# Kernel tuning notes

Hardware: AMD Instinct MI355X
Metric: run time of the kernel (lower is better)

## Reference

```python
import jax, jax.numpy as jnp
import numpy as np

ORDER = 12      # Coef_num in the original
BLOCK = 1024
N_FFT = 2046    # torch.stft(n_fft=2046) -> 1024 onesided bins
HOP = 511       # torch default n_fft // 4
WORN = 1024
G1, G2 = 0.92, 0.6


def burg_lpc(y):
    """Burg's method LPC (exactly librosa.lpc), vectorized over blocks. y: [B, N] -> [B, ORDER+1]."""
    ar = jnp.zeros((y.shape[0], ORDER + 1), y.dtype).at[:, 0].set(1.0)
    f = y[:, 1:]
    b = y[:, :-1]
    den = jnp.sum(f * f, -1) + jnp.sum(b * b, -1)
    for i in range(ORDER):
        k = -2.0 * jnp.sum(b * f, -1) / den                     # reflection coeff [B]
        js = np.arange(1, i + 2)
        ar = ar.at[:, js].set(ar[:, js] + k[:, None] * ar[:, i - js + 1])
        f_new = f + k[:, None] * b
        b = b + k[:, None] * f
        f = f_new
        den = (1.0 - k * k) * den - b[:, -1] ** 2 - f[:, 0] ** 2
        f = f[:, 1:]
        b = b[:, :-1]
    return ar


def perceptual_weights(y):
    """Stacked |freqz| weight matrix [n_blocks*11, 1024], matching the original append order."""
    n_blocks = y.shape[0] // BLOCK
    yb = y[: n_blocks * BLOCK].reshape(n_blocks, BLOCK)
    lpc = burg_lpc(yb)[:, :ORDER]                               # original drops coeff index 12
    j = np.arange(ORDER)
    a1 = (lpc * (G1 ** j)).astype(jnp.complex64)                # denominator coeffs (bandwidth-expanded)
    a2 = (lpc * (G2 ** j)).astype(jnp.complex64)                # numerator coeffs
    omega = jnp.pi * jnp.arange(WORN) / WORN                    # freqz worN=1024 digital freqs
    E = jnp.exp(-1j * omega[:, None] * j[None, :]).astype(jnp.complex64)   # [F, 12]
    # freqz is called inside the k1 loop: at step k1 only coeffs 0..k1 are filled -> triangular mask
    M = jnp.asarray(j[None, :] <= np.arange(1, ORDER)[:, None], jnp.complex64)  # [11, 12]
    num = jnp.einsum('bj,kj,fj->bkf', a2, M, E)
    den = jnp.einsum('bj,kj,fj->bkf', a1, M, E)
    return jnp.abs(num / den).reshape(n_blocks * (ORDER - 1), WORN)


def stft_mag(x):
    """torch.stft(x, n_fft=2046, center=True, reflect pad, rect window, onesided) magnitude -> [1024, n_frames]."""
    pad = N_FFT // 2
    xp = jnp.pad(x, (pad, pad), mode='reflect')
    n_frames = 1 + x.shape[0] // HOP
    idx = jnp.arange(n_frames)[:, None] * HOP + jnp.arange(N_FFT)[None, :]
    frames = xp[idx]                                            # [n_frames, 2046]
    return jnp.abs(jnp.fft.rfft(frames, axis=1)).T              # [1024, n_frames]


def setup_inputs() -> dict:
    key = jax.random.key(0)
    kx, ky = jax.random.split(key)
    L = 2048 * 1024
    x = jax.random.normal(kx, (L,), dtype=jnp.float32)
    y = jax.random.normal(ky, (L,), dtype=jnp.float32)
    return {"x": x, "y": y}


def reference(x, y):
    W = jax.lax.stop_gradient(perceptual_weights(y))            # original computes weights on detached numpy
    Sx = stft_mag(x)
    Sy = stft_mag(y)
    mse = jnp.mean((Sx - Sy) ** 2, axis=1)                      # [1024] per-frequency-bin MSE over frames
    return jnp.mean(mse[None, :] / W)                           # broadcast over [n_blocks*11, 1024]
```

## Files before the change

kernel.cpp:

```cpp
#include <hip/hip_runtime.h>
#include <hip/hip_bf16.h>

#define PI_D 3.14159265358979323846
#define L_TOTAL 2097152
#define NFRAMES 4105
#define NBLK    4108
#define MROWS_P 8216
#define MPAD    8320
#define KP      512
#define NDIM    2048
#define PSTRIDE 8224


#define FRAMES_BLOCKS 2080
#define BASIS_BLOCKS  512
#define SARR_BLOCKS   17
#define BURG_BLOCKS   512
#define PREP_BLOCKS   (FRAMES_BLOCKS + BASIS_BLOCKS + SARR_BLOCKS + BURG_BLOCKS)

typedef __attribute__((ext_vector_type(8))) short short8;
typedef __attribute__((ext_vector_type(4))) short short4v;
typedef __attribute__((ext_vector_type(4))) float floatx4;

typedef __attribute__((address_space(1))) void gvoid_as1;
typedef __attribute__((address_space(3))) void lvoid_as3;

__device__ __forceinline__ void gld_lds16(const void* g, void* l) {
    __builtin_amdgcn_global_load_lds((gvoid_as1*)g, (lvoid_as3*)l, 16, 0, 0);
}

__device__ __forceinline__ float b2f(short v) {
    unsigned int u = ((unsigned int)(unsigned short)v) << 16;
    return __uint_as_float(u);
}

__device__ __forceinline__ float xorall(float v) {
    v += __shfl_xor(v, 1, 64);
    v += __shfl_xor(v, 2, 64);
    v += __shfl_xor(v, 4, 64);
    v += __shfl_xor(v, 8, 64);
    v += __shfl_xor(v, 16, 64);
    v += __shfl_xor(v, 32, 64);
    return v;
}

__device__ __forceinline__ float wave_reduce(float v) {
    v += __shfl_down(v, 32, 64);
    v += __shfl_down(v, 16, 64);
    v += __shfl_down(v, 8, 64);
    v += __shfl_down(v, 4, 64);
    v += __shfl_down(v, 2, 64);
    v += __shfl_down(v, 1, 64);
    return v;
}

__device__ __forceinline__ void frames_body(int bid, int tid,
                                            const float* __restrict__ x,
                                            const float* __restrict__ y,
                                            __hip_bfloat16* __restrict__ A) {
    const int ci = bid * 256 + tid;
    const int rb = ci >> 10;
    const int kc = (ci >> 4) & 63;
    const int rowIn = ci & 15;
    const int row = rb * 16 + rowIn;
    __hip_bfloat16 tmp[8];
    if (row < MROWS_P) {
        const int b = row >> 1;
        const float* src = (row & 1) ? y : x;
        const int base = b * 511 + kc * 8 - 1023;
#pragma unroll
        for (int e = 0; e < 8; e++) {
            const int n = kc * 8 + e;
            float v = 0.f;
            if (n < 511) {
                int p = base + e;
                if (p < 0) p = -p;
                else if (p >= L_TOTAL) p = 2 * L_TOTAL - 2 - p;
                v = src[p];
            }
            tmp[e] = __float2bfloat16(v);
        }
    } else {
#pragma unroll
        for (int e = 0; e < 8; e++) tmp[e] = __float2bfloat16(0.f);
    }
    *(short8*)((char*)A + (size_t)ci * 16) = *(short8*)tmp;
}

__device__ __forceinline__ void basis_body(int bid, int tid,
                                           __hip_bfloat16* __restrict__ Bt) {
    const int ci = bid * 256 + tid;
    const int rb = ci >> 10;
    const int kc = (ci >> 4) & 63;
    const int rowIn = ci & 15;
    const int row = rb * 16 + rowIn;
    const int f = row >> 1;
    const bool isSin = row & 1;
    __hip_bfloat16 tmp[8];
#pragma unroll
    for (int e = 0; e < 8; e++) {
        const int n = kc * 8 + e;
        float v = 0.f;
        if (n < 511) {
            const int m = (f * n) % 2046;
            const float ang = (float)m * (float)(PI_D / 1023.0);
            float s, c;
            __sincosf(ang, &s, &c);
            v = isSin ? -s : c;
        }
        tmp[e] = __float2bfloat16(v);
    }
    *(short8*)((char*)Bt + (size_t)ci * 16) = *(short8*)tmp;
}

__device__ __forceinline__ void sarr_body(int bid, int tid,
                                          const float* __restrict__ x,
                                          const float* __restrict__ y,
                                          float4* __restrict__ S) {
    const int b = bid * 256 + tid;
    int p0 = 511 * b - 1023;
    int p1 = p0 + 1;
    int m0 = (p0 < 0) ? -p0 : ((p0 >= L_TOTAL) ? 2 * L_TOTAL - 2 - p0 : p0);
    int m1 = (p1 < 0) ? -p1 : ((p1 >= L_TOTAL) ? 2 * L_TOTAL - 2 - p1 : p1);
    S[b] = make_float4(x[m0], x[m1], y[m0], y[m1]);
}

__device__ __forceinline__ void burg_body(int bid, int tid,
                                          const float* __restrict__ y,
                                          float* __restrict__ ar_out,
                                          float* __restrict__ wsf) {
    if (bid < 8) wsf[bid * 256 + tid] = 0.f;

    const int lane = tid & 63;
    const int wid = tid >> 6;
    const int blk = bid * 4 + wid;
    const float4* yb4 = (const float4*)(y + (size_t)blk * 1024) + lane * 4;

    float t[16];
#pragma unroll
    for (int q = 0; q < 4; q++) {
        float4 v = yb4[q];
        t[q * 4 + 0] = v.x; t[q * 4 + 1] = v.y;
        t[q * 4 + 2] = v.z; t[q * 4 + 3] = v.w;
    }
    float b[16], f[16];
#pragma unroll
    for (int r = 0; r < 16; r++) b[r] = t[r];
#pragma unroll
    for (int r = 0; r < 15; r++) f[r] = t[r + 1];
    {
        float nb = __shfl_down(t[0], 1, 64);
        f[15] = (lane == 63) ? 0.f : nb;
        if (lane == 63) b[15] = 0.f;
    }

    float den = 0.f;
#pragma unroll
    for (int r = 0; r < 16; r++) den += f[r] * f[r] + b[r] * b[r];
    den = xorall(den);

    float ar_s[13];
    ar_s[0] = 1.f;
#pragma unroll
    for (int j = 1; j < 13; j++) ar_s[j] = 0.f;

#pragma unroll
    for (int i = 0; i < 12; i++) {
        float num = 0.f;
#pragma unroll
        for (int r = 0; r < 16; r++) num += f[r] * b[r];
        num = xorall(num);
        const float k = -2.f * num / den;

        float fu[16], bu[16];
#pragma unroll
        for (int r = 0; r < 16; r++) {
            fu[r] = f[r] + k * b[r];
            bu[r] = b[r] + k * f[r];
        }
        const float f0 = __shfl(fu[0], 0, 64);
        const int pos = 1022 - i;
        const int L = pos >> 4, S = pos & 15;
        const float blast = __shfl(bu[S], L, 64);

        den = (1.f - k * k) * den - blast * blast - f0 * f0;

        float nf = __shfl_down(fu[0], 1, 64);
#pragma unroll
        for (int r = 0; r < 15; r++) f[r] = fu[r + 1];
        f[15] = (lane == 63) ? 0.f : nf;
#pragma unroll
        for (int r = 0; r < 16; r++) b[r] = bu[r];
        if (lane == L) b[S] = 0.f;

        float tmp[13];
#pragma unroll
        for (int js = 1; js <= i + 1; js++) tmp[js] = ar_s[js] + k * ar_s[i + 1 - js];
#pragma unroll
        for (int js = 1; js <= i + 1; js++) ar_s[js] = tmp[js];
    }

#pragma unroll
    for (int j = 0; j < 12; j++)
        if (lane == j) ar_out[(size_t)blk * 12 + j] = ar_s[j];
}

__global__ __launch_bounds__(256) void prep_kernel(const float* __restrict__ x,
                                                   const float* __restrict__ y,
                                                   __hip_bfloat16* __restrict__ A,
                                                   __hip_bfloat16* __restrict__ Bt,
                                                   float4* __restrict__ S,
                                                   float* __restrict__ ar,
                                                   float* __restrict__ wsf) {
    const int bid = blockIdx.x;
    const int tid = threadIdx.x;
    if (bid < FRAMES_BLOCKS) {
        frames_body(bid, tid, x, y, A);
    } else if (bid < FRAMES_BLOCKS + BASIS_BLOCKS) {
        basis_body(bid - FRAMES_BLOCKS, tid, Bt);
    } else if (bid < FRAMES_BLOCKS + BASIS_BLOCKS + SARR_BLOCKS) {
        sarr_body(bid - FRAMES_BLOCKS - BASIS_BLOCKS, tid, x, y, S);
    } else {
        burg_body(bid - FRAMES_BLOCKS - BASIS_BLOCKS - SARR_BLOCKS, tid, y, ar, wsf);
    }
}

__global__ __launch_bounds__(256) void invw_kernel(const float* __restrict__ ar,
                                                   float* __restrict__ invW) {
    __shared__ float sar[16][12];
    const int tid = threadIdx.x;
    const int f = blockIdx.x * 256 + tid;
    const int b0 = blockIdx.y * 16;
    if (tid < 16 * 12) ((float*)sar)[tid] = ar[(size_t)b0 * 12 + tid];
    __syncthreads();

    const float omega = (float)(PI_D / 1024.0) * (float)f;
    float sw, cw;
    __sincosf(omega, &sw, &cw);

    float acc = 0.f;
#pragma unroll 4
    for (int bb = 0; bb < 16; bb++) {
        float a0 = sar[bb][0];
        float nr = a0, ni = 0.f, dr = a0, di = 0.f;
        float er = 1.f, ei = 0.f;
        float g1p = 1.f, g2p = 1.f;
#pragma unroll
        for (int j = 1; j < 12; j++) {
            float er2 = er * cw + ei * sw;
            float ei2 = ei * cw - er * sw;
            er = er2; ei = ei2;
            g1p *= 0.92f; g2p *= 0.6f;
            float aj = sar[bb][j];
            float a1 = aj * g1p, a2 = aj * g2p;
            nr += a2 * er; ni += a2 * ei;
            dr += a1 * er; di += a1 * ei;
            float D = dr * dr + di * di;
            float Nn = nr * nr + ni * ni;
            acc += D * __builtin_amdgcn_rsqf(D * Nn);
        }
    }
    atomicAdd(&invW[f], acc);
}

__global__ __launch_bounds__(256) void gemm_p_kernel(
    const __hip_bfloat16* __restrict__ A, const __hip_bfloat16* __restrict__ Bt,
    __hip_bfloat16* __restrict__ Pt) {
    __shared__ __align__(16) __hip_bfloat16 Al[128 * 32];
    __shared__ __align__(16) __hip_bfloat16 Bl[128 * 32];

    const int tid = threadIdx.x;
    const int lane = tid & 63;
    const int w = tid >> 6;
    const int wm = w >> 1, wn = w & 1;
    const int q = lane >> 4, l15 = lane & 15;
    const int tileN = blockIdx.x * 128;
    const int tileM = blockIdx.y * 128;

    floatx4 acc[4][4];
#pragma unroll
    for (int i = 0; i < 4; i++)
#pragma unroll
        for (int j = 0; j < 4; j++) acc[i][j] = (floatx4){0.f, 0.f, 0.f, 0.f};

    const int rl = tid & 15;
    const int qq = (tid >> 4) & 3;
    const int gg0 = tid >> 6;
    const char* pA0 = (const char*)A + ((((size_t)(tileM >> 4) + gg0) << 10) + qq * 16 + rl) * 16;
    const char* pA1 = pA0 + (size_t)4 * 16384;
    const char* pB0 = (const char*)Bt + ((((size_t)(tileN >> 4) + gg0) << 10) + qq * 16 + rl) * 16;
    const char* pB1 = pB0 + (size_t)4 * 16384;
    char* AlB = (char*)Al;
    char* BlB = (char*)Bl;

    for (int it = 0; it < KP / 32; it++) {
        gld_lds16(pA0, AlB + tid * 16);
        gld_lds16(pA1, AlB + (tid + 256) * 16);
        gld_lds16(pB0, BlB + tid * 16);
        gld_lds16(pB1, BlB + (tid + 256) * 16);
        pA0 += 1024; pA1 += 1024; pB0 += 1024; pB1 += 1024;
        __syncthreads();

        short8 af[4], bf[4];
#pragma unroll
        for (int sm = 0; sm < 4; sm++)
            af[sm] = *(const short8*)(AlB + (((wm * 4 + sm) * 64 + lane) * 16));
#pragma unroll
        for (int sn = 0; sn < 4; sn++)
            bf[sn] = *(const short8*)(BlB + (((wn * 4 + sn) * 64 + lane) * 16));
#pragma unroll
        for (int sm = 0; sm < 4; sm++)
#pragma unroll
            for (int sn = 0; sn < 4; sn++)
                acc[sm][sn] = __builtin_amdgcn_mfma_f32_16x16x32_bf16(
                    af[sm], bf[sn], acc[sm][sn], 0, 0, 0);
        __syncthreads();
    }

#pragma unroll
    for (int sm = 0; sm < 4; sm++) {
        const int rowBase = tileM + wm * 64 + sm * 16 + q * 4;
        if (rowBase >= MROWS_P) continue;
#pragma unroll
        for (int sn = 0; sn < 4; sn++) {
            const int colG = tileN + wn * 64 + sn * 16 + l15;
            short4v pk;
#pragma unroll
            for (int r = 0; r < 4; r++) {
                __hip_bfloat16 h = __float2bfloat16(acc[sm][sn][r]);
                pk[r] = *(short*)&h;
            }
            *(short4v*)((char*)Pt + ((size_t)colG * PSTRIDE + rowBase) * 2) = pk;
        }
    }
}

__global__ __launch_bounds__(256) void combine_kernel(
    const __hip_bfloat16* __restrict__ Pt,
    const float4* __restrict__ S,
    float* __restrict__ mse_sum) {
    const int tid = threadIdx.x;
    const int lane = tid & 63;
    const int wid = tid >> 6;
    const int f = blockIdx.x * 4 + wid;
    const int ty = blockIdx.y;

    float wc[4], ws[4];
    wc[0] = 1.f; ws[0] = 0.f;
#pragma unroll
    for (int h = 1; h < 4; h++) {
        int m = (511 * h * f) % 2046;
        float s, c;
        __sincosf((float)m * (float)(PI_D / 1023.0), &s, &c);
        wc[h] = c; ws[h] = -s;
    }
    float wtc0, wts0, wtc1, wts1;
    {
        int m = (2044 * f) % 2046;
        float s, c;
        __sincosf((float)m * (float)(PI_D / 1023.0), &s, &c);
        wtc0 = c; wts0 = -s;
        m = (2045 * f) % 2046;
        __sincosf((float)m * (float)(PI_D / 1023.0), &s, &c);
        wtc1 = c; wts1 = -s;
    }

    const __hip_bfloat16* rowRe = Pt + (size_t)(2 * f) * PSTRIDE;
    const __hip_bfloat16* rowIm = rowRe + PSTRIDE;

    float acc = 0.f;
    const int tt0 = ty * 256 + 4 * lane;
    if (tt0 < NFRAMES) {
        short8 re0 = *(const short8*)(rowRe + 2 * tt0);
        short8 re1 = *(const short8*)(rowRe + 2 * tt0 + 8);
        short8 im0 = *(const short8*)(rowIm + 2 * tt0);
        short8 im1 = *(const short8*)(rowIm + 2 * tt0 + 8);
        float4 sT[4];
#pragma unroll
        for (int d = 0; d < 4; d++) sT[d] = S[tt0 + 4 + d];
        float vr[16], vi[16];
#pragma unroll
        for (int j = 0; j < 8; j++) {
            vr[j] = b2f(re0[j]); vr[j + 8] = b2f(re1[j]);
            vi[j] = b2f(im0[j]); vi[j + 8] = b2f(im1[j]);
        }
#pragma unroll
        for (int d = 0; d < 4; d++) {
            const int tt = tt0 + d;
            if (tt >= NFRAMES) break;
            float xr = 0.f, xi = 0.f, yr = 0.f, yi = 0.f;
#pragma unroll
            for (int h = 0; h < 4; h++) {
                const int qx = 2 * d + 2 * h;
                xr += wc[h] * vr[qx] - ws[h] * vi[qx];
                xi += wc[h] * vi[qx] + ws[h] * vr[qx];
                const int qy = qx + 1;
                yr += wc[h] * vr[qy] - ws[h] * vi[qy];
                yi += wc[h] * vi[qy] + ws[h] * vr[qy];
            }
            const float4 sd = sT[d];
            xr += wtc0 * sd.x + wtc1 * sd.y;
            xi += wts0 * sd.x + wts1 * sd.y;
            yr += wtc0 * sd.z + wtc1 * sd.w;
            yi += wts0 * sd.z + wts1 * sd.w;
            float dm = sqrtf(xr * xr + xi * xi) - sqrtf(yr * yr + yi * yi);
            acc += dm * dm;
        }
    }
    acc = xorall(acc);
    if (lane == 0) atomicAdd(&mse_sum[f], acc);
}

__global__ void final_kernel(const float* __restrict__ mse_sum,
                             const float* __restrict__ invW,
                             float* __restrict__ out) {
    __shared__ float red[4];
    const int tid = threadIdx.x;
    float lo = 0.f;
    for (int f = tid; f < 1024; f += 256) lo += mse_sum[f] * invW[f];
    lo = wave_reduce(lo);
    if ((tid & 63) == 0) red[tid >> 6] = lo;
    __syncthreads();
    if (tid == 0) {
        float tot = red[0] + red[1] + red[2] + red[3];
        out[0] = tot * (float)(1.0 / (4105.0 * 22528.0 * 1024.0));
    }
}

extern "C" void kernel_launch(void* const* d_in, const int* in_sizes, int n_in,
                              void* d_out, int out_size, void* d_ws, size_t ws_size,
                              hipStream_t stream) {
    const float* x = (const float*)d_in[0];
    const float* y = (const float*)d_in[1];
    float* out = (float*)d_out;

    float* wsf = (float*)d_ws;
    float* mse_sum = wsf;
    float* invW = wsf + 1024;
    float* ar = wsf + 2048;
    float4* S = (float4*)((char*)d_ws + 106496);
    __hip_bfloat16* Ap = (__hip_bfloat16*)((char*)d_ws + 196608);
    __hip_bfloat16* Bp = (__hip_bfloat16*)((char*)d_ws + 8716288);
    __hip_bfloat16* Pt = (__hip_bfloat16*)((char*)d_ws + 10813440);

    prep_kernel<<<PREP_BLOCKS, 256, 0, stream>>>(x, y, Ap, Bp, S, ar, wsf);
    invw_kernel<<<dim3(4, 128), 256, 0, stream>>>(ar, invW);
    gemm_p_kernel<<<dim3(NDIM / 128, MPAD / 128), 256, 0, stream>>>(Ap, Bp, Pt);
    combine_kernel<<<dim3(256, 17), 256, 0, stream>>>(Pt, S, mse_sum);
    final_kernel<<<1, 256, 0, stream>>>(mse_sum, invW, out);
}
```

Baseline: 145.1 us.

## Merge invW into GEMM launch, fold final reduction into combine, cheapen basis sincos

Fuses the invw kernel into the GEMM launch as extra blocks, and replaces the final reduction kernel with a last-block-done counter pattern inside the combine kernel. Together these cut the launch count from five to three and remove small tail kernels. The basis generator now computes the twiddle factors with one sincos plus a rotation recurrence instead of eight sincos calls. The recurrence can add small rounding drift, but the values are rounded to bf16 anyway. The counter lives in the workspace and is zeroed by prep, so the workspace offsets are shifted to make room for it.

```diff
diff --git a/kernel.cpp b/kernel.cpp
--- a/kernel.cpp
+++ b/kernel.cpp
@@ -10,6 +10,10 @@
 #define KP      512
 #define NDIM    2048
 #define PSTRIDE 8224
+
+#define GEMM_BLOCKS 1040
+#define INVW_BLOCKS 512
+#define COMBINE_BLOCKS (256 * 17)
 
 
 #define FRAMES_BLOCKS 2080
@@ -96,19 +100,21 @@
     const int row = rb * 16 + rowIn;
     const int f = row >> 1;
     const bool isSin = row & 1;
+    const int n0 = kc * 8;
+    const int m0 = (f * n0) % 2046;
+    float s, c, ss, cs;
+    __sincosf((float)m0 * (float)(PI_D / 1023.0), &s, &c);
+    __sincosf((float)f * (float)(PI_D / 1023.0), &ss, &cs);
     __hip_bfloat16 tmp[8];
 #pragma unroll
     for (int e = 0; e < 8; e++) {
-        const int n = kc * 8 + e;
-        float v = 0.f;
-        if (n < 511) {
-            const int m = (f * n) % 2046;
-            const float ang = (float)m * (float)(PI_D / 1023.0);
-            float s, c;
-            __sincosf(ang, &s, &c);
-            v = isSin ? -s : c;
-        }
+        const int n = n0 + e;
+        float v = isSin ? -s : c;
+        if (n >= 511) v = 0.f;
         tmp[e] = __float2bfloat16(v);
+        float c2 = c * cs - s * ss;
+        float s2 = s * cs + c * ss;
+        c = c2; s = s2;
     }
     *(short8*)((char*)Bt + (size_t)ci * 16) = *(short8*)tmp;
 }
@@ -129,7 +135,10 @@
                                           const float* __restrict__ y,
                                           float* __restrict__ ar_out,
                                           float* __restrict__ wsf) {
-    if (bid < 8) wsf[bid * 256 + tid] = 0.f;
+    if (bid < 9) {
+        const int idx = bid * 256 + tid;
+        if (idx < 2080) wsf[idx] = 0.f;
+    }
 
     const int lane = tid & 63;
     const int wid = tid >> 6;
@@ -225,12 +234,82 @@
     }
 }
 
-__global__ __launch_bounds__(256) void invw_kernel(const float* __restrict__ ar,
-                                                   float* __restrict__ invW) {
-    __shared__ float sar[16][12];
-    const int tid = threadIdx.x;
-    const int f = blockIdx.x * 256 + tid;
-    const int b0 = blockIdx.y * 16;
+__device__ __forceinline__ void gemm_body(int bx, int by, int tid, char* smem,
+                                          const __hip_bfloat16* __restrict__ A,
+                                          const __hip_bfloat16* __restrict__ Bt,
+                                          __hip_bfloat16* __restrict__ Pt) {
+    char* AlB = smem;
+    char* BlB = smem + 8192;
+
+    const int lane = tid & 63;
+    const int w = tid >> 6;
+    const int wm = w >> 1, wn = w & 1;
+    const int q = lane >> 4, l15 = lane & 15;
+    const int tileN = bx * 128;
+    const int tileM = by * 128;
+
+    floatx4 acc[4][4];
+#pragma unroll
+    for (int i = 0; i < 4; i++)
+#pragma unroll
+        for (int j = 0; j < 4; j++) acc[i][j] = (floatx4){0.f, 0.f, 0.f, 0.f};
+
+    const int rl = tid & 15;
+    const int qq = (tid >> 4) & 3;
+    const int gg0 = tid >> 6;
+    const char* pA0 = (const char*)A + ((((size_t)(tileM >> 4) + gg0) << 10) + qq * 16 + rl) * 16;
+    const char* pA1 = pA0 + (size_t)4 * 16384;
+    const char* pB0 = (const char*)Bt + ((((size_t)(tileN >> 4) + gg0) << 10) + qq * 16 + rl) * 16;
+    const char* pB1 = pB0 + (size_t)4 * 16384;
+
+    for (int it = 0; it < KP / 32; it++) {
+        gld_lds16(pA0, AlB + tid * 16);
+        gld_lds16(pA1, AlB + (tid + 256) * 16);
+        gld_lds16(pB0, BlB + tid * 16);
+        gld_lds16(pB1, BlB + (tid + 256) * 16);
+        pA0 += 1024; pA1 += 1024; pB0 += 1024; pB1 += 1024;
+        __syncthreads();
+
+        short8 af[4], bf[4];
+#pragma unroll
+        for (int sm = 0; sm < 4; sm++)
+            af[sm] = *(const short8*)(AlB + (((wm * 4 + sm) * 64 + lane) * 16));
+#pragma unroll
+        for (int sn = 0; sn < 4; sn++)
+            bf[sn] = *(const short8*)(BlB + (((wn * 4 + sn) * 64 + lane) * 16));
+#pragma unroll
+        for (int sm = 0; sm < 4; sm++)
+#pragma unroll
+            for (int sn = 0; sn < 4; sn++)
+                acc[sm][sn] = __builtin_amdgcn_mfma_f32_16x16x32_bf16(
+                    af[sm], bf[sn], acc[sm][sn], 0, 0, 0);
+        __syncthreads();
+    }
+
+#pragma unroll
+    for (int sm = 0; sm < 4; sm++) {
+        const int rowBase = tileM + wm * 64 + sm * 16 + q * 4;
+        if (rowBase >= MROWS_P) continue;
+#pragma unroll
+        for (int sn = 0; sn < 4; sn++) {
+            const int colG = tileN + wn * 64 + sn * 16 + l15;
+            short4v pk;
+#pragma unroll
+            for (int r = 0; r < 4; r++) {
+                __hip_bfloat16 h = __float2bfloat16(acc[sm][sn][r]);
+                pk[r] = *(short*)&h;
+            }
+            *(short4v*)((char*)Pt + ((size_t)colG * PSTRIDE + rowBase) * 2) = pk;
+        }
+    }
+}
+
+__device__ __forceinline__ void invw_body(int bid, int tid, char* smem,
+                                          const float* __restrict__ ar,
+                                          float* __restrict__ invW) {
+    float (*sar)[12] = (float(*)[12])smem;
+    const int f = (bid & 3) * 256 + tid;
+    const int b0 = (bid >> 2) * 16;
     if (tid < 16 * 12) ((float*)sar)[tid] = ar[(size_t)b0 * 12 + tid];
     __syncthreads();
 
@@ -263,82 +342,27 @@
     atomicAdd(&invW[f], acc);
 }
 
-__global__ __launch_bounds__(256) void gemm_p_kernel(
+__global__ __launch_bounds__(256) void gemm_invw_kernel(
     const __hip_bfloat16* __restrict__ A, const __hip_bfloat16* __restrict__ Bt,
-    __hip_bfloat16* __restrict__ Pt) {
-    __shared__ __align__(16) __hip_bfloat16 Al[128 * 32];
-    __shared__ __align__(16) __hip_bfloat16 Bl[128 * 32];
-
+    __hip_bfloat16* __restrict__ Pt,
+    const float* __restrict__ ar, float* __restrict__ invW) {
+    __shared__ __align__(16) char smem[16384];
+    const int bid = blockIdx.x;
     const int tid = threadIdx.x;
-    const int lane = tid & 63;
-    const int w = tid >> 6;
-    const int wm = w >> 1, wn = w & 1;
-    const int q = lane >> 4, l15 = lane & 15;
-    const int tileN = blockIdx.x * 128;
-    const int tileM = blockIdx.y * 128;
-
-    floatx4 acc[4][4];
-#pragma unroll
-    for (int i = 0; i < 4; i++)
-#pragma unroll
-        for (int j = 0; j < 4; j++) acc[i][j] = (floatx4){0.f, 0.f, 0.f, 0.f};
-
-    const int rl = tid & 15;
-    const int qq = (tid >> 4) & 3;
-    const int gg0 = tid >> 6;
-    const char* pA0 = (const char*)A + ((((size_t)(tileM >> 4) + gg0) << 10) + qq * 16 + rl) * 16;
-    const char* pA1 = pA0 + (size_t)4 * 16384;
-    const char* pB0 = (const char*)Bt + ((((size_t)(tileN >> 4) + gg0) << 10) + qq * 16 + rl) * 16;
-    const char* pB1 = pB0 + (size_t)4 * 16384;
-    char* AlB = (char*)Al;
-    char* BlB = (char*)Bl;
-
-    for (int it = 0; it < KP / 32; it++) {
-        gld_lds16(pA0, AlB + tid * 16);
-        gld_lds16(pA1, AlB + (tid + 256) * 16);
-        gld_lds16(pB0, BlB + tid * 16);
-        gld_lds16(pB1, BlB + (tid + 256) * 16);
-        pA0 += 1024; pA1 += 1024; pB0 += 1024; pB1 += 1024;
-        __syncthreads();
-
-        short8 af[4], bf[4];
-#pragma unroll
-        for (int sm = 0; sm < 4; sm++)
-            af[sm] = *(const short8*)(AlB + (((wm * 4 + sm) * 64 + lane) * 16));
-#pragma unroll
-        for (int sn = 0; sn < 4; sn++)
-            bf[sn] = *(const short8*)(BlB + (((wn * 4 + sn) * 64 + lane) * 16));
-#pragma unroll
-        for (int sm = 0; sm < 4; sm++)
-#pragma unroll
-            for (int sn = 0; sn < 4; sn++)
-                acc[sm][sn] = __builtin_amdgcn_mfma_f32_16x16x32_bf16(
-                    af[sm], bf[sn], acc[sm][sn], 0, 0, 0);
-        __syncthreads();
-    }
-
-#pragma unroll
-    for (int sm = 0; sm < 4; sm++) {
-        const int rowBase = tileM + wm * 64 + sm * 16 + q * 4;
-        if (rowBase >= MROWS_P) continue;
-#pragma unroll
-        for (int sn = 0; sn < 4; sn++) {
-            const int colG = tileN + wn * 64 + sn * 16 + l15;
-            short4v pk;
-#pragma unroll
-            for (int r = 0; r < 4; r++) {
-                __hip_bfloat16 h = __float2bfloat16(acc[sm][sn][r]);
-                pk[r] = *(short*)&h;
-            }
-            *(short4v*)((char*)Pt + ((size_t)colG * PSTRIDE + rowBase) * 2) = pk;
-        }
+    if (bid < GEMM_BLOCKS) {
+        gemm_body(bid & 15, bid >> 4, tid, smem, A, Bt, Pt);
+    } else {
+        invw_body(bid - GEMM_BLOCKS, tid, smem, ar, invW);
     }
 }
 
 __global__ __launch_bounds__(256) void combine_kernel(
     const __hip_bfloat16* __restrict__ Pt,
     const float4* __restrict__ S,
-    float* __restrict__ mse_sum) {
+    float* __restrict__ mse_sum,
+    const float* __restrict__ invW,
+    int* __restrict__ cnt,
+    float* __restrict__ out) {
     const int tid = threadIdx.x;
     const int lane = tid & 63;
     const int wid = tid >> 6;
@@ -409,21 +433,30 @@
     }
     acc = xorall(acc);
     if (lane == 0) atomicAdd(&mse_sum[f], acc);
-}
-
-__global__ void final_kernel(const float* __restrict__ mse_sum,
-                             const float* __restrict__ invW,
-                             float* __restrict__ out) {
-    __shared__ float red[4];
-    const int tid = threadIdx.x;
-    float lo = 0.f;
-    for (int f = tid; f < 1024; f += 256) lo += mse_sum[f] * invW[f];
-    lo = wave_reduce(lo);
-    if ((tid & 63) == 0) red[tid >> 6] = lo;
+
+    __threadfence();
     __syncthreads();
+    __shared__ int isLast;
     if (tid == 0) {
-        float tot = red[0] + red[1] + red[2] + red[3];
-        out[0] = tot * (float)(1.0 / (4105.0 * 22528.0 * 1024.0));
+        int old = __hip_atomic_fetch_add(cnt, 1, __ATOMIC_ACQ_REL, __HIP_MEMORY_SCOPE_AGENT);
+        isLast = (old == COMBINE_BLOCKS - 1) ? 1 : 0;
+    }
+    __syncthreads();
+    if (isLast) {
+        __shared__ float red[4];
+        float lo = 0.f;
+        for (int ff = tid; ff < 1024; ff += 256) {
+            float ms = __hip_atomic_load(&mse_sum[ff], __ATOMIC_RELAXED, __HIP_MEMORY_SCOPE_AGENT);
+            float iw = __hip_atomic_load((float*)&invW[ff], __ATOMIC_RELAXED, __HIP_MEMORY_SCOPE_AGENT);
+            lo += ms * iw;
+        }
+        lo = wave_reduce(lo);
+        if ((tid & 63) == 0) red[tid >> 6] = lo;
+        __syncthreads();
+        if (tid == 0) {
+            float tot = red[0] + red[1] + red[2] + red[3];
+            out[0] = tot * (float)(1.0 / (4105.0 * 22528.0 * 1024.0));
+        }
     }
 }
 
@@ -437,15 +470,14 @@
     float* wsf = (float*)d_ws;
     float* mse_sum = wsf;
     float* invW = wsf + 1024;
-    float* ar = wsf + 2048;
-    float4* S = (float4*)((char*)d_ws + 106496);
-    __hip_bfloat16* Ap = (__hip_bfloat16*)((char*)d_ws + 196608);
-    __hip_bfloat16* Bp = (__hip_bfloat16*)((char*)d_ws + 8716288);
-    __hip_bfloat16* Pt = (__hip_bfloat16*)((char*)d_ws + 10813440);
+    int* cnt = (int*)(wsf + 2048);
+    float* ar = wsf + 2080;
+    float4* S = (float4*)((char*)d_ws + 131072);
+    __hip_bfloat16* Ap = (__hip_bfloat16*)((char*)d_ws + 262144);
+    __hip_bfloat16* Bp = (__hip_bfloat16*)((char*)d_ws + 8781824);
+    __hip_bfloat16* Pt = (__hip_bfloat16*)((char*)d_ws + 10878976);
 
     prep_kernel<<<PREP_BLOCKS, 256, 0, stream>>>(x, y, Ap, Bp, S, ar, wsf);
-    invw_kernel<<<dim3(4, 128), 256, 0, stream>>>(ar, invW);
-    gemm_p_kernel<<<dim3(NDIM / 128, MPAD / 128), 256, 0, stream>>>(Ap, Bp, Pt);
-    combine_kernel<<<dim3(256, 17), 256, 0, stream>>>(Pt, S, mse_sum);
-    final_kernel<<<1, 256, 0, stream>>>(mse_sum, invW, out);
-}
+    gemm_invw_kernel<<<GEMM_BLOCKS + INVW_BLOCKS, 256, 0, stream>>>(Ap, Bp, Pt, ar, invW);
+    combine_kernel<<<dim3(256, 17), 256, 0, stream>>>(Pt, S, mse_sum, invW, cnt, out);
+}
```

Result: slower. 514.7 us (+254.6%).
